# Kernel tuning notes

Hardware: AMD Instinct MI355X
Metric: run time of the kernel (lower is better)

The kernel has to match this reference:

```python
import jax, jax.numpy as jnp
from jax import lax
import numpy as np

ALPHA, BETA, DECAY, GAMMA = 0.9, 0.1, 0.9, 0.5
KW = 5  # temporal_window


def setup_inputs() -> dict:
    key = jax.random.key(0)
    k1, k2 = jax.random.split(key)
    B, T, F = 128, 128, 2048
    x = jax.random.normal(k1, (B, T, F), dtype=jnp.float32)
    init_threshold = jnp.array(1.0, dtype=jnp.float32)
    conv_w = jax.random.normal(k2, (1, 1, KW), dtype=jnp.float32) * 0.2  # Conv1d(1,1,KW) weight
    conv_b = jnp.zeros((1,), dtype=jnp.float32)
    spatial_attn = jnp.array([1.0], dtype=jnp.float32)
    return {"x": x, "init_threshold": init_threshold, "conv_w": conv_w,
            "conv_b": conv_b, "spatial_attn": spatial_attn}


def _forward(x, init_threshold, conv_w, conv_b, spatial_attn):
    B, T, F = x.shape
    # --- temporal encoding: Conv1d(1,1,KW,'same') along time, per (batch,feature) ---
    xt = jnp.transpose(x, (0, 2, 1)).reshape(B * F, 1, T)  # [B*F,1,T]
    conv = lax.conv_general_dilated(xt, conv_w, window_strides=(1,), padding='SAME',
                                    dimension_numbers=('NCH', 'OIH', 'NCH'))
    conv = conv + conv_b[None, :, None]
    x = jnp.transpose(conv.reshape(B, F, T), (0, 2, 1))  # [B,T,F]
    # --- spatial attention ---
    w = jax.nn.sigmoid(spatial_attn * x.mean(axis=1, keepdims=True))  # [B,1,F]
    x = x * (1.0 + GAMMA * w)
    # --- LIF recurrence over time ---
    mem0 = jnp.zeros((B, F), dtype=x.dtype)
    thr0 = jnp.broadcast_to(init_threshold, (B, F)).astype(x.dtype)
    hist0 = jnp.zeros((B, 3, F), dtype=x.dtype)
    pi = jnp.float32(np.pi)

    def step(carry, xt):
        mem, thr, hist = carry
        mem = DECAY * mem + xt
        spike = 0.5 * (jnp.arctan(pi * (mem - thr) / 2) / pi + 0.5)  # multi_atan surrogate
        hist = jnp.concatenate([hist[:, 1:], spike[:, None]], axis=1)  # [B,3,F]
        avg = hist.mean(axis=1)  # [B,F]
        new_thr = ALPHA * thr + (1.0 - ALPHA) * init_threshold + BETA * avg
        mem = mem - spike * lax.stop_gradient(new_thr)
        return (mem, new_thr, hist), spike

    (mem, _, _), spikes = lax.scan(step, (mem0, thr0, hist0), jnp.transpose(x, (1, 0, 2)))
    return jnp.transpose(spikes, (1, 0, 2)), mem  # [B,T,F], [B,F]


def reference(x, init_threshold, conv_w, conv_b, spatial_attn):
    return _forward(x, init_threshold, conv_w, conv_b, spatial_attn)
```

## Files before the change

### kernel.cpp

```cpp
#include <hip/hip_runtime.h>
#include <math.h>

constexpr int B = 128, T = 128, F = 2048, KW = 5;
#define ALPHA 0.9f
#define BETA  0.1f
#define DECAY 0.9f
#define GAMMA 0.5f

__global__ __launch_bounds__(256) void lif_fused_kernel(
    const float* __restrict__ x,
    const float* __restrict__ thr0p,
    const float* __restrict__ convw,
    const float* __restrict__ convb,
    const float* __restrict__ sattn,
    float* __restrict__ out)
{
    const int tid = blockIdx.x * blockDim.x + threadIdx.x;
    const int f   = tid & (F - 1);
    const int b   = tid >> 11;

    const float w0 = convw[0], w1 = convw[1], w2 = convw[2],
                w3 = convw[3], w4 = convw[4];
    const float cb   = convb[0];
    const float thr0 = thr0p[0];
    const float sa   = sattn[0];

    const float* xp = x + (size_t)b * T * F + f;

    float s0 = 0.f, s1 = 0.f, s2 = 0.f, s3 = 0.f;
#pragma unroll 4
    for (int t = 0; t < T; t += 4) {
        s0 += xp[(size_t)(t + 0) * F];
        s1 += xp[(size_t)(t + 1) * F];
        s2 += xp[(size_t)(t + 2) * F];
        s3 += xp[(size_t)(t + 3) * F];
    }
    const float sx = (s0 + s1) + (s2 + s3);

    const float e0  = xp[0];
    const float e1  = xp[(size_t)F];
    const float em2 = xp[(size_t)(T - 2) * F];
    const float em1 = xp[(size_t)(T - 1) * F];

    const float W = ((w0 + w1) + (w2 + w3)) + w4;
    const float csum = fmaf(W, sx, (float)T * cb)
                     - (w3 + w4) * e0 - w4 * e1 - w0 * em2 - (w0 + w1) * em1;

    const float z     = sa * (csum * (1.0f / (float)T));
    const float watt  = 1.0f / (1.0f + expf(-z));
    const float scale = 1.0f + GAMMA * watt;

    const float PI  = 3.14159265358979323846f;
    const float thc = (1.0f - ALPHA) * thr0;

    float mem = 0.f, thr = thr0;
    float h0 = 0.f, h1 = 0.f, h2 = 0.f;
    float a = 0.f, bb = 0.f, c = e0, d = e1;

    float* sp = out + (size_t)b * T * F + f;
    float* mp = out + (size_t)B * T * F + (size_t)b * F + f;

    auto lif_step = [&](int t, float e) {
        float ct = fmaf(w0, a, fmaf(w1, bb, fmaf(w2, c,
                   fmaf(w3, d, fmaf(w4, e, cb)))));
        mem = fmaf(DECAY, mem, ct * scale);
        float sarg  = PI * (mem - thr) * 0.5f;
        float spike = 0.5f * (atanf(sarg) * (1.0f / PI) + 0.5f);
        h0 = h1; h1 = h2; h2 = spike;
        float avg = (h0 + h1 + h2) * (1.0f / 3.0f);
        thr = fmaf(ALPHA, thr, fmaf(BETA, avg, thc));
        mem = fmaf(-spike, thr, mem);
        __builtin_nontemporal_store(spike, sp + (size_t)t * F);
        a = bb; bb = c; c = d; d = e;
    };

#pragma unroll 8
    for (int t = 0; t < T - 2; ++t) {
        float e = xp[(size_t)(t + 2) * F];
        lif_step(t, e);
    }
    lif_step(T - 2, 0.f);
    lif_step(T - 1, 0.f);

    __builtin_nontemporal_store(mem, mp);
}

extern "C" void kernel_launch(void* const* d_in, const int* in_sizes, int n_in,
                              void* d_out, int out_size, void* d_ws, size_t ws_size,
                              hipStream_t stream) {
    const float* x     = (const float*)d_in[0];
    const float* thr0  = (const float*)d_in[1];
    const float* convw = (const float*)d_in[2];
    const float* convb = (const float*)d_in[3];
    const float* sattn = (const float*)d_in[4];
    float* out = (float*)d_out;

    const int total = B * F;
    const int block = 256;
    const int grid  = total / block;

    lif_fused_kernel<<<grid, block, 0, stream>>>(x, thr0, convw, convb, sattn, out);
}
```

Before: 264.5 us.

## Double-buffer time-chunk loads into LDS via global_load_lds and use polynomial atan

```diff
diff --git a/kernel.cpp b/kernel.cpp
--- a/kernel.cpp
+++ b/kernel.cpp
@@ -7,7 +7,34 @@
 #define DECAY 0.9f
 #define GAMMA 0.5f
 
-__global__ __launch_bounds__(256) void lif_fused_kernel(
+constexpr int TG  = 16;
+constexpr int NG  = T / TG;
+constexpr int BLK = 256;
+
+__device__ __forceinline__ void load_lds16(const float* gsrc, float* lds) {
+    __builtin_amdgcn_global_load_lds(
+        (const __attribute__((address_space(1))) unsigned int*)gsrc,
+        (__attribute__((address_space(3))) unsigned int*)lds,
+        16, 0, 0);
+}
+
+__device__ __forceinline__ float atan_fast(float z) {
+    float az  = __builtin_fabsf(z);
+    float inv = __builtin_amdgcn_rcpf(az);
+    bool  big = az > 1.0f;
+    float u   = big ? inv : az;
+    float u2  = u * u;
+    float p   = fmaf(u2, -0.01172120f, 0.05265332f);
+    p = fmaf(u2, p, -0.11643287f);
+    p = fmaf(u2, p,  0.19354346f);
+    p = fmaf(u2, p, -0.33262347f);
+    p = fmaf(u2, p,  0.99997726f);
+    float r = u * p;
+    r = big ? (1.57079632679f - r) : r;
+    return copysignf(r, z);
+}
+
+__global__ __launch_bounds__(256, 4) void lif_fused_kernel(
     const float* __restrict__ x,
     const float* __restrict__ thr0p,
     const float* __restrict__ convw,
@@ -15,9 +42,13 @@
     const float* __restrict__ sattn,
     float* __restrict__ out)
 {
-    const int tid = blockIdx.x * blockDim.x + threadIdx.x;
-    const int f   = tid & (F - 1);
-    const int b   = tid >> 11;
+    const int b    = blockIdx.x >> 3;
+    const int f0   = (blockIdx.x & 7) * BLK;
+    const int fg   = f0 + threadIdx.x;
+    const int lane = threadIdx.x & 63;
+    const int wid  = threadIdx.x >> 6;
+
+    __shared__ float buf[2][TG][BLK];
 
     const float w0 = convw[0], w1 = convw[1], w2 = convw[2],
                 w3 = convw[3], w4 = convw[4];
@@ -25,62 +56,84 @@
     const float thr0 = thr0p[0];
     const float sa   = sattn[0];
 
-    const float* xp = x + (size_t)b * T * F + f;
+    const float* xbase = x + (size_t)b * T * F;
+    const float* xp    = xbase + fg;
 
-    float s0 = 0.f, s1 = 0.f, s2 = 0.f, s3 = 0.f;
-#pragma unroll 4
-    for (int t = 0; t < T; t += 4) {
-        s0 += xp[(size_t)(t + 0) * F];
-        s1 += xp[(size_t)(t + 1) * F];
-        s2 += xp[(size_t)(t + 2) * F];
-        s3 += xp[(size_t)(t + 3) * F];
+    float s0=0.f,s1=0.f,s2=0.f,s3=0.f,s4=0.f,s5=0.f,s6=0.f,s7=0.f;
+#pragma unroll 2
+    for (int t = 0; t < T; t += 8) {
+        s0 += xp[(size_t)(t+0)*F]; s1 += xp[(size_t)(t+1)*F];
+        s2 += xp[(size_t)(t+2)*F]; s3 += xp[(size_t)(t+3)*F];
+        s4 += xp[(size_t)(t+4)*F]; s5 += xp[(size_t)(t+5)*F];
+        s6 += xp[(size_t)(t+6)*F]; s7 += xp[(size_t)(t+7)*F];
     }
-    const float sx = (s0 + s1) + (s2 + s3);
+    const float sx = ((s0+s1)+(s2+s3)) + ((s4+s5)+(s6+s7));
 
     const float e0  = xp[0];
     const float e1  = xp[(size_t)F];
-    const float em2 = xp[(size_t)(T - 2) * F];
-    const float em1 = xp[(size_t)(T - 1) * F];
+    const float em2 = xp[(size_t)(T-2)*F];
+    const float em1 = xp[(size_t)(T-1)*F];
 
-    const float W = ((w0 + w1) + (w2 + w3)) + w4;
+    const float W = ((w0+w1)+(w2+w3)) + w4;
     const float csum = fmaf(W, sx, (float)T * cb)
-                     - (w3 + w4) * e0 - w4 * e1 - w0 * em2 - (w0 + w1) * em1;
+                     - (w3+w4)*e0 - w4*e1 - w0*em2 - (w0+w1)*em1;
 
-    const float z     = sa * (csum * (1.0f / (float)T));
+    const float z     = sa * (csum * (1.0f/(float)T));
     const float watt  = 1.0f / (1.0f + expf(-z));
     const float scale = 1.0f + GAMMA * watt;
 
-    const float PI  = 3.14159265358979323846f;
-    const float thc = (1.0f - ALPHA) * thr0;
+    const float PIH    = 1.57079632679f;
+    const float INV2PI = 0.15915494309f;
+    const float thc    = (1.0f - ALPHA) * thr0;
 
     float mem = 0.f, thr = thr0;
-    float h0 = 0.f, h1 = 0.f, h2 = 0.f;
+    float h1 = 0.f, h2 = 0.f;
     float a = 0.f, bb = 0.f, c = e0, d = e1;
 
-    float* sp = out + (size_t)b * T * F + f;
-    float* mp = out + (size_t)B * T * F + (size_t)b * F + f;
+    float* sp = out + (size_t)b * T * F + fg;
+    float* mp = out + (size_t)B * T * F + (size_t)b * F + fg;
+
+    auto stage = [&](int g, int pb) {
+#pragma unroll
+        for (int r4 = 0; r4 < 4; ++r4) {
+            const int row = (wid << 2) | r4;
+            const int te  = g * TG + 2 + row;
+            if (te < T)
+                load_lds16(xbase + (size_t)te * F + f0 + (lane << 2),
+                           &buf[pb][row][0]);
+        }
+        if (g == NG - 1) {
+            buf[pb][TG-2][threadIdx.x] = 0.0f;
+            buf[pb][TG-1][threadIdx.x] = 0.0f;
+        }
+    };
 
     auto lif_step = [&](int t, float e) {
         float ct = fmaf(w0, a, fmaf(w1, bb, fmaf(w2, c,
                    fmaf(w3, d, fmaf(w4, e, cb)))));
         mem = fmaf(DECAY, mem, ct * scale);
-        float sarg  = PI * (mem - thr) * 0.5f;
-        float spike = 0.5f * (atanf(sarg) * (1.0f / PI) + 0.5f);
-        h0 = h1; h1 = h2; h2 = spike;
-        float avg = (h0 + h1 + h2) * (1.0f / 3.0f);
+        float sarg  = PIH * (mem - thr);
+        float spike = fmaf(atan_fast(sarg), INV2PI, 0.25f);
+        float avg   = (h1 + h2 + spike) * (1.0f/3.0f);
+        h1 = h2; h2 = spike;
         thr = fmaf(ALPHA, thr, fmaf(BETA, avg, thc));
         mem = fmaf(-spike, thr, mem);
         __builtin_nontemporal_store(spike, sp + (size_t)t * F);
         a = bb; bb = c; c = d; d = e;
     };
 
-#pragma unroll 8
-    for (int t = 0; t < T - 2; ++t) {
-        float e = xp[(size_t)(t + 2) * F];
-        lif_step(t, e);
+    stage(0, 0);
+    __syncthreads();
+    for (int g = 0; g < NG; ++g) {
+        if (g + 1 < NG) stage(g + 1, (g + 1) & 1);
+        const int pb = g & 1;
+#pragma unroll
+        for (int r = 0; r < TG; ++r) {
+            float e = buf[pb][r][threadIdx.x];
+            lif_step(g * TG + r, e);
+        }
+        __syncthreads();
     }
-    lif_step(T - 2, 0.f);
-    lif_step(T - 1, 0.f);
 
     __builtin_nontemporal_store(mem, mp);
 }
@@ -95,9 +148,6 @@
     const float* sattn = (const float*)d_in[4];
     float* out = (float*)d_out;
 
-    const int total = B * F;
-    const int block = 256;
-    const int grid  = total / block;
-
-    lif_fused_kernel<<<grid, block, 0, stream>>>(x, thr0, convw, convb, sattn, out);
+    const int grid = B * (F / BLK);
+    lif_fused_kernel<<<grid, BLK, 0, stream>>>(x, thr0, convw, convb, sattn, out);
 }
```

Measured after the change: 262.2 us. No clear change (-0.9%).
